# Kernel optimization log

Hardware: AMD Instinct MI355X
Metric: run time of the kernel (lower is better)

The kernel has to match this reference:

```python
import jax, jax.numpy as jnp
import numpy as np

N_NODE = 50000
N_EDGE = 800000
D = 64       # in_dim = out_dim = hidden_dim
A = 64       # attn_dim
N_REL = 475  # 2*237+1 relation ids
B = 32       # batch of queries


def setup_inputs() -> dict:
    key = jax.random.key(0)
    ks = jax.random.split(key, 16)
    hidden = jax.random.normal(ks[0], (N_NODE, D), dtype=jnp.float32)
    sub = jax.random.randint(ks[1], (N_EDGE,), 0, N_NODE)
    rel = jax.random.randint(ks[2], (N_EDGE,), 0, N_REL)
    obj = jax.random.randint(ks[3], (N_EDGE,), 0, N_NODE)
    edges = jnp.stack([sub, rel, obj], axis=1)  # [E, 3]
    gnn_emb_rel = jax.random.normal(ks[4], (N_REL, D), dtype=jnp.float32)
    mapping = jax.random.randint(ks[5], (N_REL,), 0, N_REL)  # rel id -> unique-rel row
    q_rel = jax.random.randint(ks[6], (B,), 0, N_REL)
    r_idx = jax.random.randint(ks[7], (N_EDGE,), 0, B)  # edge -> query index
    s = 1.0 / np.sqrt(D)
    sa = 1.0 / np.sqrt(A)
    u = lambda k, shape, b: jax.random.uniform(k, shape, jnp.float32, minval=-b, maxval=b)
    return {
        "hidden": hidden,
        "edges": edges,
        "gnn_emb_rel": gnn_emb_rel,
        "mapping": mapping,
        "q_rel": q_rel,
        "r_idx": r_idx,
        "n_node": N_NODE,
        "Ws_w": u(ks[8], (A, D), s),
        "Wr_w": u(ks[9], (A, D), s),
        "Wqr_w": u(ks[10], (A, D), s),
        "Wqr_b": u(ks[11], (A,), s),
        "walpha_w": u(ks[12], (1, A), sa),
        "walpha_b": u(ks[13], (1,), sa),
        "Wh_w": u(ks[14], (D, D), s),
    }


def reference(hidden, edges, gnn_emb_rel, mapping, q_rel, r_idx, n_node,
              Ws_w, Wr_w, Wqr_w, Wqr_b, walpha_w, walpha_b, Wh_w):
    sub, rel, obj = edges[:, 0], edges[:, 1], edges[:, 2]
    hs = hidden[sub]                       # [E, D] gather
    hr = gnn_emb_rel[mapping[rel]]         # [E, D] gather
    # per-query h_qr projected once, then gathered per edge (same math, cheaper)
    hq = gnn_emb_rel[mapping[q_rel]]       # [B, D]
    qr_attn = hq @ Wqr_w.T + Wqr_b         # [B, A]
    pre = hs @ Ws_w.T + hr @ Wr_w.T + qr_attn[r_idx]   # [E, A]
    alpha = jax.nn.sigmoid(jax.nn.relu(pre) @ walpha_w.T + walpha_b)  # [E, 1]
    message = alpha * (hs * hr)            # [E, D]
    message_agg = jax.ops.segment_sum(message, obj, num_segments=n_node)  # [N, D]
    hidden_new = jax.nn.relu(message_agg @ Wh_w.T)  # act = ReLU from GNN_auto
    return hidden_new
```

## Files before the change

kernel.cpp:

```cpp
#include <hip/hip_runtime.h>
#include <hip/hip_bf16.h>

#define D64 64
#define WTP 65

__device__ inline float lane_bcast(float v, int l) {
    return __uint_as_float(__builtin_amdgcn_readlane(__float_as_uint(v), l));
}
__device__ inline float bf16_lo(unsigned u) { return __uint_as_float(u << 16); }
__device__ inline float bf16_hi(unsigned u) { return __uint_as_float(u & 0xFFFF0000u); }
__device__ inline float bf16u(unsigned short u) { return __uint_as_float((unsigned)u << 16); }
__device__ inline unsigned short f2bf(float f) {
    __hip_bfloat16 b = __float2bfloat16(f);
    return *(unsigned short*)&b;
}

__global__ void rowmm_bf16_hist_kernel(const float* __restrict__ in, const float* __restrict__ W,
                                       unsigned short* __restrict__ outb,
                                       unsigned short* __restrict__ inb, int nrows,
                                       const int* __restrict__ edges, const int* __restrict__ r_idx,
                                       int* __restrict__ counts, uint2* __restrict__ epack,
                                       int E) {
    __shared__ float WT[D64 * WTP];
    int tid = threadIdx.x;
    for (int i = tid; i < D64 * D64; i += blockDim.x)
        WT[(i & 63) * WTP + (i >> 6)] = W[i];
    __syncthreads();
    int lane = tid & 63;
    int wid = (blockIdx.x * blockDim.x + tid) >> 6;
    int nw = (gridDim.x * blockDim.x) >> 6;
    for (int r = wid; r < nrows; r += nw) {
        float v = in[r * D64 + lane];
        inb[r * D64 + lane] = f2bf(v);
        float acc = 0.f;
#pragma unroll
        for (int d = 0; d < D64; ++d)
            acc = fmaf(lane_bcast(v, d), WT[d * WTP + lane], acc);
        outb[r * D64 + lane] = f2bf(acc);
    }
    int gt = blockIdx.x * blockDim.x + tid;
    int gs = gridDim.x * blockDim.x;
    for (int i = gt; i < E; i += gs) {
        int sub = edges[i * 3 + 0];
        int rel = edges[i * 3 + 1];
        int obj = edges[i * 3 + 2];
        int ri  = r_idx[i];
        epack[i] = make_uint2((unsigned)sub | ((unsigned)rel << 17) | ((unsigned)ri << 26),
                              (unsigned)obj);
        atomicAdd(&counts[obj], 1);
    }
}

__global__ void prep_kernel(const float* __restrict__ emb, const int* __restrict__ mapping,
                            const int* __restrict__ q_rel,
                            const float* __restrict__ Wr, const float* __restrict__ Wqr,
                            const float* __restrict__ Wqr_b,
                            unsigned short* __restrict__ hrmapb,
                            unsigned short* __restrict__ hrWb,
                            unsigned short* __restrict__ qrb, int nrel, int nq) {
    int b = blockIdx.x;
    int lane = threadIdx.x;
    if (b < nrel) {
        int m = mapping[b];
        float v = emb[m * D64 + lane];
        hrmapb[b * D64 + lane] = f2bf(v);
        float acc = 0.f;
#pragma unroll
        for (int d = 0; d < D64; ++d)
            acc = fmaf(lane_bcast(v, d), Wr[lane * D64 + d], acc);
        hrWb[b * D64 + lane] = f2bf(acc);
    } else {
        int q = b - nrel;
        if (q < nq) {
            int m = mapping[q_rel[q]];
            float v = emb[m * D64 + lane];
            float acc = Wqr_b[lane];
#pragma unroll
            for (int d = 0; d < D64; ++d)
                acc = fmaf(lane_bcast(v, d), Wqr[lane * D64 + d], acc);
            qrb[q * D64 + lane] = f2bf(acc);
        }
    }
}

__global__ void scan1_kernel(const int* __restrict__ counts, int* __restrict__ offs,
                             int* __restrict__ partials, int n) {
    __shared__ int tsum[256];
    int t = threadIdx.x;
    int base = blockIdx.x * 1024 + t * 4;
    int v[4];
    int s = 0;
#pragma unroll
    for (int i = 0; i < 4; ++i) {
        int idx = base + i;
        int c = (idx < n) ? counts[idx] : 0;
        v[i] = s;
        s += c;
    }
    tsum[t] = s;
    __syncthreads();
    for (int off = 1; off < 256; off <<= 1) {
        int y = (t >= off) ? tsum[t - off] : 0;
        __syncthreads();
        tsum[t] += y;
        __syncthreads();
    }
    int incl = tsum[t];
    int thread_prefix = incl - s;
    if (t == 255) partials[blockIdx.x] = incl;
#pragma unroll
    for (int i = 0; i < 4; ++i) {
        int idx = base + i;
        if (idx < n) offs[idx] = thread_prefix + v[i];
    }
}

__global__ void scan2_kernel(int* partials, int nb) {
    int t = threadIdx.x;
    int own = (t < nb) ? partials[t] : 0;
    int v = own;
    for (int off = 1; off < 64; off <<= 1) {
        int y = __shfl_up(v, off, 64);
        if (t >= off) v += y;
    }
    if (t < nb) partials[t] = v - own;
}

__global__ void scan3_kernel(int* __restrict__ offs, const int* __restrict__ partials, int n) {
    int base = blockIdx.x * 1024 + threadIdx.x;
    int add = partials[blockIdx.x];
#pragma unroll
    for (int i = 0; i < 4; ++i) {
        int idx = base + i * 256;
        if (idx < n) offs[idx] += add;
    }
}

__global__ void alpha_scatter_kernel(const uint2* __restrict__ epack,
                                     const unsigned short* __restrict__ hsWb,
                                     const unsigned short* __restrict__ hrWb,
                                     const unsigned short* __restrict__ qrb,
                                     const float* __restrict__ walpha_w,
                                     const float* __restrict__ walpha_b,
                                     int* __restrict__ offs, int2* __restrict__ rec,
                                     int E, int half) {
    int tid = blockIdx.x * blockDim.x + threadIdx.x;
    int e0 = tid >> 3;
    int l = tid & 7;
    if (e0 >= half) return;
    int e1 = e0 + half;
    bool has1 = (e1 < E);

    uint2 p0 = epack[e0];
    uint2 p1 = has1 ? epack[e1] : make_uint2(0u, 0u);
    int sub0 = p0.x & 0x1FFFF, rel0 = (p0.x >> 17) & 0x1FF, ri0 = p0.x >> 26, obj0 = (int)p0.y;
    int sub1 = p1.x & 0x1FFFF, rel1 = (p1.x >> 17) & 0x1FF, ri1 = p1.x >> 26, obj1 = (int)p1.y;

    uint4 hv0 = *(const uint4*)(hsWb + (size_t)sub0 * D64 + l * 8);
    uint4 rv0 = *(const uint4*)(hrWb + (size_t)rel0 * D64 + l * 8);
    uint4 qv0 = *(const uint4*)(qrb  + (size_t)ri0  * D64 + l * 8);
    uint4 hv1 = *(const uint4*)(hsWb + (size_t)sub1 * D64 + l * 8);
    uint4 rv1 = *(const uint4*)(hrWb + (size_t)rel1 * D64 + l * 8);
    uint4 qv1 = *(const uint4*)(qrb  + (size_t)ri1  * D64 + l * 8);
    const float4* w = (const float4*)(walpha_w + l * 8);
    float4 w0 = w[0], w1 = w[1];

    float x0, x1;
    x0 = fmaxf(bf16_lo(hv0.x) + bf16_lo(rv0.x) + bf16_lo(qv0.x), 0.f) * w0.x;
    x0 = fmaf(fmaxf(bf16_hi(hv0.x) + bf16_hi(rv0.x) + bf16_hi(qv0.x), 0.f), w0.y, x0);
    x0 = fmaf(fmaxf(bf16_lo(hv0.y) + bf16_lo(rv0.y) + bf16_lo(qv0.y), 0.f), w0.z, x0);
    x0 = fmaf(fmaxf(bf16_hi(hv0.y) + bf16_hi(rv0.y) + bf16_hi(qv0.y), 0.f), w0.w, x0);
    x0 = fmaf(fmaxf(bf16_lo(hv0.z) + bf16_lo(rv0.z) + bf16_lo(qv0.z), 0.f), w1.x, x0);
    x0 = fmaf(fmaxf(bf16_hi(hv0.z) + bf16_hi(rv0.z) + bf16_hi(qv0.z), 0.f), w1.y, x0);
    x0 = fmaf(fmaxf(bf16_lo(hv0.w) + bf16_lo(rv0.w) + bf16_lo(qv0.w), 0.f), w1.z, x0);
    x0 = fmaf(fmaxf(bf16_hi(hv0.w) + bf16_hi(rv0.w) + bf16_hi(qv0.w), 0.f), w1.w, x0);

    x1 = fmaxf(bf16_lo(hv1.x) + bf16_lo(rv1.x) + bf16_lo(qv1.x), 0.f) * w0.x;
    x1 = fmaf(fmaxf(bf16_hi(hv1.x) + bf16_hi(rv1.x) + bf16_hi(qv1.x), 0.f), w0.y, x1);
    x1 = fmaf(fmaxf(bf16_lo(hv1.y) + bf16_lo(rv1.y) + bf16_lo(qv1.y), 0.f), w0.z, x1);
    x1 = fmaf(fmaxf(bf16_hi(hv1.y) + bf16_hi(rv1.y) + bf16_hi(qv1.y), 0.f), w0.w, x1);
    x1 = fmaf(fmaxf(bf16_lo(hv1.z) + bf16_lo(rv1.z) + bf16_lo(qv1.z), 0.f), w1.x, x1);
    x1 = fmaf(fmaxf(bf16_hi(hv1.z) + bf16_hi(rv1.z) + bf16_hi(qv1.z), 0.f), w1.y, x1);
    x1 = fmaf(fmaxf(bf16_lo(hv1.w) + bf16_lo(rv1.w) + bf16_lo(qv1.w), 0.f), w1.z, x1);
    x1 = fmaf(fmaxf(bf16_hi(hv1.w) + bf16_hi(rv1.w) + bf16_hi(qv1.w), 0.f), w1.w, x1);

    x0 += __shfl_xor(x0, 4, 64);
    x1 += __shfl_xor(x1, 4, 64);
    x0 += __shfl_xor(x0, 2, 64);
    x1 += __shfl_xor(x1, 2, 64);
    x0 += __shfl_xor(x0, 1, 64);
    x1 += __shfl_xor(x1, 1, 64);

    if (l == 0) {
        float wb = walpha_b[0];
        float a0 = 1.f / (1.f + __expf(-(x0 + wb)));
        int slot0 = atomicAdd(&offs[obj0], 1);
        rec[slot0] = make_int2(sub0 | (rel0 << 17), __float_as_int(a0));
        if (has1) {
            float a1 = 1.f / (1.f + __expf(-(x1 + wb)));
            int slot1 = atomicAdd(&offs[obj1], 1);
            rec[slot1] = make_int2(sub1 | (rel1 << 17), __float_as_int(a1));
        }
    }
}

__global__ void agg_wh_kernel(const int2* __restrict__ rec, const int* __restrict__ endoff,
                              const unsigned short* __restrict__ hiddenb,
                              const unsigned short* __restrict__ hrmapb,
                              const float* __restrict__ Wh,
                              float* __restrict__ out, int NN) {
    __shared__ float WT[D64 * WTP];
    int tid = threadIdx.x;
    for (int i = tid; i < D64 * D64; i += blockDim.x)
        WT[(i & 63) * WTP + (i >> 6)] = Wh[i];
    __syncthreads();
    int lane = tid & 63;
    int n = (blockIdx.x * blockDim.x + tid) >> 6;
    if (n >= NN) return;
    int start = (n == 0) ? 0 : endoff[n - 1];
    int end = endoff[n];
    start = __builtin_amdgcn_readfirstlane(start);
    end = __builtin_amdgcn_readfirstlane(end);
    float acc0 = 0.f, acc1 = 0.f, acc2 = 0.f, acc3 = 0.f;
    for (int base = start; base < end; base += 64) {
        int cnt = end - base;
        if (cnt > 64) cnt = 64;
        int rx = 0, ry = 0;
        if (lane < cnt) {
            int2 r = rec[base + lane];
            rx = r.x; ry = r.y;
        }
        int j = 0;
        for (; j + 3 < cnt; j += 4) {
            int rx0 = __builtin_amdgcn_readlane(rx, j);
            int ry0 = __builtin_amdgcn_readlane(ry, j);
            int rx1 = __builtin_amdgcn_readlane(rx, j + 1);
            int ry1 = __builtin_amdgcn_readlane(ry, j + 1);
            int rx2 = __builtin_amdgcn_readlane(rx, j + 2);
            int ry2 = __builtin_amdgcn_readlane(ry, j + 2);
            int rx3 = __builtin_amdgcn_readlane(rx, j + 3);
            int ry3 = __builtin_amdgcn_readlane(ry, j + 3);
            float h0 = bf16u(hiddenb[(size_t)(rx0 & 0x1FFFF) * D64 + lane]);
            float m0 = bf16u(hrmapb[(size_t)((unsigned)rx0 >> 17) * D64 + lane]);
            float h1 = bf16u(hiddenb[(size_t)(rx1 & 0x1FFFF) * D64 + lane]);
            float m1 = bf16u(hrmapb[(size_t)((unsigned)rx1 >> 17) * D64 + lane]);
            float h2 = bf16u(hiddenb[(size_t)(rx2 & 0x1FFFF) * D64 + lane]);
            float m2 = bf16u(hrmapb[(size_t)((unsigned)rx2 >> 17) * D64 + lane]);
            float h3 = bf16u(hiddenb[(size_t)(rx3 & 0x1FFFF) * D64 + lane]);
            float m3 = bf16u(hrmapb[(size_t)((unsigned)rx3 >> 17) * D64 + lane]);
            acc0 = fmaf(__uint_as_float(ry0) * h0, m0, acc0);
            acc1 = fmaf(__uint_as_float(ry1) * h1, m1, acc1);
            acc2 = fmaf(__uint_as_float(ry2) * h2, m2, acc2);
            acc3 = fmaf(__uint_as_float(ry3) * h3, m3, acc3);
        }
        for (; j < cnt; ++j) {
            int rx0 = __builtin_amdgcn_readlane(rx, j);
            int ry0 = __builtin_amdgcn_readlane(ry, j);
            float h0 = bf16u(hiddenb[(size_t)(rx0 & 0x1FFFF) * D64 + lane]);
            float m0 = bf16u(hrmapb[(size_t)((unsigned)rx0 >> 17) * D64 + lane]);
            acc0 = fmaf(__uint_as_float(ry0) * h0, m0, acc0);
        }
    }
    float acc = (acc0 + acc1) + (acc2 + acc3);
    float o = 0.f;
#pragma unroll
    for (int d = 0; d < D64; ++d)
        o = fmaf(lane_bcast(acc, d), WT[d * WTP + lane], o);
    out[(size_t)n * D64 + lane] = fmaxf(o, 0.f);
}

extern "C" void kernel_launch(void* const* d_in, const int* in_sizes, int n_in,
                              void* d_out, int out_size, void* d_ws, size_t ws_size,
                              hipStream_t stream) {
    const float* hidden   = (const float*)d_in[0];
    const int*   edges    = (const int*)d_in[1];
    const float* emb_rel  = (const float*)d_in[2];
    const int*   mapping  = (const int*)d_in[3];
    const int*   q_rel    = (const int*)d_in[4];
    const int*   r_idx    = (const int*)d_in[5];
    const float* Ws_w     = (const float*)d_in[7];
    const float* Wr_w     = (const float*)d_in[8];
    const float* Wqr_w    = (const float*)d_in[9];
    const float* Wqr_b    = (const float*)d_in[10];
    const float* walpha_w = (const float*)d_in[11];
    const float* walpha_b = (const float*)d_in[12];
    const float* Wh_w     = (const float*)d_in[13];
    float* out = (float*)d_out;

    int NN   = in_sizes[0] / D64;
    int E    = in_sizes[5];
    int NREL = in_sizes[3];
    int NQ   = in_sizes[4];

    char* ws = (char*)d_ws;
    size_t off = 0;
    unsigned short* hsWb    = (unsigned short*)(ws + off); off += (size_t)NN * D64 * 2;
    unsigned short* hiddenb = (unsigned short*)(ws + off); off += (size_t)NN * D64 * 2;
    int2*  rec  = (int2*)(ws + off);       off += (size_t)E * sizeof(int2);
    uint2* epack = (uint2*)(ws + off);     off += (size_t)E * sizeof(uint2);
    int* counts = (int*)(ws + off);        off += (size_t)NN * sizeof(int);
    int* offs   = (int*)(ws + off);        off += (size_t)NN * sizeof(int);
    int* partials = (int*)(ws + off);      off += 64 * sizeof(int);
    unsigned short* hrmapb = (unsigned short*)(ws + off); off += (size_t)NREL * D64 * 2;
    unsigned short* hrWb   = (unsigned short*)(ws + off); off += (size_t)NREL * D64 * 2;
    unsigned short* qrb    = (unsigned short*)(ws + off); off += (size_t)NQ * D64 * 2;

    int NB = (NN + 1023) / 1024;

    hipMemsetAsync(counts, 0, (size_t)NN * sizeof(int), stream);
    prep_kernel<<<NREL + NQ, 64, 0, stream>>>(emb_rel, mapping, q_rel, Wr_w, Wqr_w, Wqr_b,
                                              hrmapb, hrWb, qrb, NREL, NQ);
    rowmm_bf16_hist_kernel<<<1024, 256, 0, stream>>>(hidden, Ws_w, hsWb, hiddenb, NN,
                                                     edges, r_idx, counts, epack, E);
    scan1_kernel<<<NB, 256, 0, stream>>>(counts, offs, partials, NN);
    scan2_kernel<<<1, 64, 0, stream>>>(partials, NB);
    scan3_kernel<<<NB, 256, 0, stream>>>(offs, partials, NN);
    {
        int half = (E + 1) / 2;
        long long threads = (long long)half * 8;
        int blocks = (int)((threads + 255) / 256);
        alpha_scatter_kernel<<<blocks, 256, 0, stream>>>(epack, hsWb, hrWb, qrb,
                                                         walpha_w, walpha_b, offs, rec, E, half);
    }
    agg_wh_kernel<<<(NN * 64 + 1023) / 1024, 1024, 0, stream>>>(rec, offs, hiddenb, hrmapb,
                                                                Wh_w, out, NN);
}
```

Measured before the change: 154.5 us.

## Compute hidden@Ws projection with bf16 MFMA and split histogram into own kernel

```diff
diff --git a/kernel.cpp b/kernel.cpp
--- a/kernel.cpp
+++ b/kernel.cpp
@@ -3,6 +3,10 @@
 
 #define D64 64
 #define WTP 65
+#define LPAD 72
+
+typedef __attribute__((ext_vector_type(8))) short short8;
+typedef __attribute__((ext_vector_type(4))) float f32x4;
 
 __device__ inline float lane_bcast(float v, int l) {
     return __uint_as_float(__builtin_amdgcn_readlane(__float_as_uint(v), l));
@@ -15,30 +19,64 @@
     return *(unsigned short*)&b;
 }
 
-__global__ void rowmm_bf16_hist_kernel(const float* __restrict__ in, const float* __restrict__ W,
-                                       unsigned short* __restrict__ outb,
-                                       unsigned short* __restrict__ inb, int nrows,
-                                       const int* __restrict__ edges, const int* __restrict__ r_idx,
-                                       int* __restrict__ counts, uint2* __restrict__ epack,
-                                       int E) {
-    __shared__ float WT[D64 * WTP];
+__global__ void cvtW_kernel(const float* __restrict__ W, unsigned short* __restrict__ WsB) {
+    int i = blockIdx.x * blockDim.x + threadIdx.x;
+    if (i < D64 * D64) WsB[i] = f2bf(W[i]);
+}
+
+__global__ void rowmm_mfma_kernel(const float* __restrict__ in,
+                                  const unsigned short* __restrict__ WsB,
+                                  unsigned short* __restrict__ outb,
+                                  unsigned short* __restrict__ inb, int nrows) {
+    __shared__ unsigned short ldsA[4][16 * LPAD];
     int tid = threadIdx.x;
-    for (int i = tid; i < D64 * D64; i += blockDim.x)
-        WT[(i & 63) * WTP + (i >> 6)] = W[i];
-    __syncthreads();
     int lane = tid & 63;
+    int wv = tid >> 6;
     int wid = (blockIdx.x * blockDim.x + tid) >> 6;
-    int nw = (gridDim.x * blockDim.x) >> 6;
-    for (int r = wid; r < nrows; r += nw) {
-        float v = in[r * D64 + lane];
-        inb[r * D64 + lane] = f2bf(v);
-        float acc = 0.f;
-#pragma unroll
-        for (int d = 0; d < D64; ++d)
-            acc = fmaf(lane_bcast(v, d), WT[d * WTP + lane], acc);
-        outb[r * D64 + lane] = f2bf(acc);
-    }
-    int gt = blockIdx.x * blockDim.x + tid;
+    int rbase = wid * 16;
+    if (rbase >= nrows) return;
+
+    short8 bfrag[8];
+#pragma unroll
+    for (int t = 0; t < 4; ++t)
+#pragma unroll
+        for (int kk = 0; kk < 2; ++kk)
+            bfrag[t * 2 + kk] = *(const short8*)(WsB + (size_t)(t * 16 + (lane & 15)) * D64 +
+                                                 kk * 32 + (lane >> 4) * 8);
+
+    unsigned short* la = &ldsA[wv][0];
+#pragma unroll
+    for (int rr = 0; rr < 16; ++rr) {
+        float v = in[(size_t)(rbase + rr) * D64 + lane];
+        unsigned short b = f2bf(v);
+        inb[(size_t)(rbase + rr) * D64 + lane] = b;
+        la[rr * LPAD + lane] = b;
+    }
+
+    f32x4 acc[4];
+#pragma unroll
+    for (int t = 0; t < 4; ++t) acc[t] = (f32x4){0.f, 0.f, 0.f, 0.f};
+#pragma unroll
+    for (int kk = 0; kk < 2; ++kk) {
+        short8 afrag = *(const short8*)(la + (lane & 15) * LPAD + kk * 32 + (lane >> 4) * 8);
+#pragma unroll
+        for (int t = 0; t < 4; ++t)
+            acc[t] = __builtin_amdgcn_mfma_f32_16x16x32_bf16(afrag, bfrag[t * 2 + kk],
+                                                             acc[t], 0, 0, 0);
+    }
+#pragma unroll
+    for (int t = 0; t < 4; ++t)
+#pragma unroll
+        for (int reg = 0; reg < 4; ++reg) {
+            int row = rbase + (lane >> 4) * 4 + reg;
+            int col = t * 16 + (lane & 15);
+            outb[(size_t)row * D64 + col] = f2bf(acc[t][reg]);
+        }
+}
+
+__global__ void hist_pack_kernel(const int* __restrict__ edges, const int* __restrict__ r_idx,
+                                 int* __restrict__ counts, uint2* __restrict__ epack, int E) {
+    int gt = blockIdx.x * blockDim.x + threadIdx.x;
     int gs = gridDim.x * blockDim.x;
     for (int i = gt; i < E; i += gs) {
         int sub = edges[i * 3 + 0];
@@ -304,14 +342,20 @@
     unsigned short* hrmapb = (unsigned short*)(ws + off); off += (size_t)NREL * D64 * 2;
     unsigned short* hrWb   = (unsigned short*)(ws + off); off += (size_t)NREL * D64 * 2;
     unsigned short* qrb    = (unsigned short*)(ws + off); off += (size_t)NQ * D64 * 2;
+    unsigned short* WsB    = (unsigned short*)(ws + off); off += (size_t)D64 * D64 * 2;
 
     int NB = (NN + 1023) / 1024;
 
     hipMemsetAsync(counts, 0, (size_t)NN * sizeof(int), stream);
+    cvtW_kernel<<<(D64 * D64 + 255) / 256, 256, 0, stream>>>(Ws_w, WsB);
     prep_kernel<<<NREL + NQ, 64, 0, stream>>>(emb_rel, mapping, q_rel, Wr_w, Wqr_w, Wqr_b,
                                               hrmapb, hrWb, qrb, NREL, NQ);
-    rowmm_bf16_hist_kernel<<<1024, 256, 0, stream>>>(hidden, Ws_w, hsWb, hiddenb, NN,
-                                                     edges, r_idx, counts, epack, E);
+    {
+        int waves = (NN + 15) / 16;
+        int blocks = (waves * 64 + 255) / 256;
+        rowmm_mfma_kernel<<<blocks, 256, 0, stream>>>(hidden, WsB, hsWb, hiddenb, NN);
+    }
+    hist_pack_kernel<<<2048, 256, 0, stream>>>(edges, r_idx, counts, epack, E);
     scan1_kernel<<<NB, 256, 0, stream>>>(counts, offs, partials, NN);
     scan2_kernel<<<1, 64, 0, stream>>>(partials, NB);
     scan3_kernel<<<NB, 256, 0, stream>>>(offs, partials, NN);
```

Measured after the change: 157.2 us. Within noise of the previous version (+1.8%).
